# Kernel optimization log

Measured on AMD Instinct MI355X. Metric: run time of the kernel, lower is better.

Reference implementation:

```python
import jax, jax.numpy as jnp
import numpy as np

N = 100000
E = 3200000
IN_DIM = 128
HD = 64
HEADS = 4
NEG_SLOPE = 0.2


def setup_inputs() -> dict:
    key = jax.random.key(0)
    ks = jax.random.split(key, 12)
    s = lambda fan_in: 1.0 / np.sqrt(fan_in)
    x = jax.random.normal(ks[0], (N, IN_DIM), dtype=jnp.float32)
    edge_index = jax.random.randint(ks[1], (2, E), 0, N, dtype=jnp.int64)
    W1 = jax.random.normal(ks[2], (IN_DIM, HEADS * HD), dtype=jnp.float32) * s(IN_DIM)
    a_src1 = jax.random.normal(ks[3], (HEADS, HD), dtype=jnp.float32) * s(HD)
    a_dst1 = jax.random.normal(ks[4], (HEADS, HD), dtype=jnp.float32) * s(HD)
    b1 = jnp.zeros((HEADS * HD,), dtype=jnp.float32)
    W2 = jax.random.normal(ks[5], (HEADS * HD, HD), dtype=jnp.float32) * s(HEADS * HD)
    a_src2 = jax.random.normal(ks[6], (1, HD), dtype=jnp.float32) * s(HD)
    a_dst2 = jax.random.normal(ks[7], (1, HD), dtype=jnp.float32) * s(HD)
    b2 = jnp.zeros((HD,), dtype=jnp.float32)
    lin_w = jax.random.normal(ks[8], (HD, 2), dtype=jnp.float32) * s(HD)
    lin_b = jnp.zeros((2,), dtype=jnp.float32)
    return {"x": x, "edge_index": edge_index, "W1": W1, "a_src1": a_src1,
            "a_dst1": a_dst1, "b1": b1, "W2": W2, "a_src2": a_src2,
            "a_dst2": a_dst2, "b2": b2, "lin_w": lin_w, "lin_b": lin_b}


def gat_conv(x, src, dst, W, a_src, a_dst, bias, heads, out_dim, concat):
    n = x.shape[0]
    h = (x @ W).reshape(n, heads, out_dim)                 # [N,H,D]
    alpha_s = jnp.einsum('nhd,hd->nh', h, a_src)           # [N,H]
    alpha_d = jnp.einsum('nhd,hd->nh', h, a_dst)           # [N,H]
    e = alpha_s[src] + alpha_d[dst]                        # [Etot,H]
    e = jnp.where(e > 0, e, NEG_SLOPE * e)                 # leaky relu
    m = jax.ops.segment_max(e, dst, num_segments=n)        # scatter-softmax (stable)
    m = jnp.where(jnp.isfinite(m), m, 0.0)
    e = jnp.exp(e - m[dst])
    denom = jax.ops.segment_sum(e, dst, num_segments=n)
    alpha = e / denom[dst]                                 # [Etot,H]
    out = jax.ops.segment_sum(h[src] * alpha[:, :, None], dst, num_segments=n)  # [N,H,D]
    out = out.reshape(n, heads * out_dim) if concat else out.mean(axis=1)
    return out + bias


def reference(x, edge_index, W1, a_src1, a_dst1, b1, W2, a_src2, a_dst2, b2, lin_w, lin_b):
    n = x.shape[0]
    loops = jnp.arange(n, dtype=edge_index.dtype)
    src = jnp.concatenate([edge_index[0], loops])          # add self-loops (PyG default)
    dst = jnp.concatenate([edge_index[1], loops])
    h = gat_conv(x, src, dst, W1, a_src1, a_dst1, b1, HEADS, HD, True)
    h = jax.nn.elu(h)
    h = gat_conv(h, src, dst, W2, a_src2, a_dst2, b2, 1, HD, True)
    h = jax.nn.elu(h)
    return h @ lin_w + lin_b                               # [N,2]
```

## Files before the change

### kernel.cpp

```cpp
#include <hip/hip_runtime.h>
#include <hip/hip_fp16.h>
#include <math.h>

#define NN 100000
#define EE 3200000
#define ETOT (EE + NN)
#define NEG_SLOPE 0.2f
#define DMAX 96
#define CHUNK 4096
#define NB0 ((ETOT + CHUNK - 1) / CHUNK)
#define RB 391
#define CAP 16384

typedef _Float16 half8 __attribute__((ext_vector_type(8)));
typedef _Float16 half4v __attribute__((ext_vector_type(4)));
typedef float floatx4 __attribute__((ext_vector_type(4)));

__device__ __forceinline__ float wsum64(float v) {
#pragma unroll
  for (int o = 32; o; o >>= 1) v += __shfl_xor(v, o);
  return v;
}
__device__ __forceinline__ float lrelu(float v) { return v > 0.f ? v : NEG_SLOPE * v; }
__device__ __forceinline__ float elu1(float v) { return v > 0.f ? v : expm1f(v); }

__global__ void k_init(int* __restrict__ ccur) {
  ccur[threadIdx.x] = threadIdx.x * CAP;
}

__global__ __launch_bounds__(256) void k_pass1(const int* __restrict__ ei,
                                               int* __restrict__ ccur,
                                               unsigned* __restrict__ ebuf,
                                               const float* __restrict__ W1,
                                               const float* __restrict__ W2,
                                               _Float16* __restrict__ W1t,
                                               _Float16* __restrict__ W2t) {
  int b = blockIdx.x;
  if (b >= NB0) {
    int idx = (b - NB0) * 256 + threadIdx.x;
    if (idx < 32768) {
      int n = idx >> 7, k = idx & 127;
      W1t[idx] = (_Float16)W1[k * 256 + n];
    } else {
      int j = idx - 32768;
      int n = j >> 8, k = j & 255;
      W2t[j] = (_Float16)W2[k * 64 + n];
    }
    return;
  }
  __shared__ unsigned vv[CHUNK];
  __shared__ unsigned short cbv[CHUNK];
  __shared__ int h[256];
  __shared__ int cur[256];
  int t = threadIdx.x;
  h[t] = 0;
  __syncthreads();
  int base = b * CHUNK;
  int lim = base + CHUNK; if (lim > ETOT) lim = ETOT;
  int cnt = lim - base;
  for (int i = t; i < cnt; i += 256) {
    int e = base + i;
    int s, d;
    if (e < EE) { s = ei[e]; d = ei[EE + e]; } else { s = e - EE; d = s; }
    unsigned cb = (unsigned)d / (unsigned)RB;
    unsigned dloc = (unsigned)d - cb * (unsigned)RB;
    vv[i] = (dloc << 17) | (unsigned)s;
    cbv[i] = (unsigned short)cb;
    atomicAdd(&h[cb], 1);
  }
  __syncthreads();
  if (h[t]) cur[t] = atomicAdd(&ccur[t], h[t]);
  __syncthreads();
  for (int i = t; i < cnt; i += 256) {
    int cb = cbv[i];
    int pos = atomicAdd(&cur[cb], 1);
    ebuf[pos] = vv[i];
  }
}

__global__ __launch_bounds__(256) void k_pass2(const unsigned* __restrict__ ebuf,
                                               const int* __restrict__ ccur,
                                               int* __restrict__ offs,
                                               int* __restrict__ degarr,
                                               int* __restrict__ csr) {
  __shared__ unsigned ed[CAP];
  __shared__ int hist[RB];
  __shared__ int cur[RB];
  int b = blockIdx.x, t = threadIdx.x;
  int d0 = b * RB;
  int rb = NN - d0; if (rb > RB) rb = RB;
  int w0 = b * CAP;
  int cnt = ccur[b] - w0;
  if (cnt > CAP) cnt = CAP;
  for (int j = t; j < rb; j += 256) hist[j] = 0;
  __syncthreads();
  for (int i = t; i < cnt; i += 256) {
    unsigned v = ebuf[w0 + i];
    ed[i] = v;
    atomicAdd(&hist[v >> 17], 1);
  }
  __syncthreads();
  if (t == 0) {
    int run = w0;
    for (int j = 0; j < rb; ++j) { cur[j] = run; run += hist[j]; }
  }
  __syncthreads();
  for (int j = t; j < rb; j += 256) {
    offs[d0 + j] = cur[j];
    degarr[d0 + j] = hist[j];
  }
  __syncthreads();
  for (int i = t; i < cnt; i += 256) {
    unsigned v = ed[i];
    int pos = atomicAdd(&cur[v >> 17], 1);
    csr[pos] = (int)(v & 0x1FFFFu);
  }
}

__global__ __launch_bounds__(256) void k_gemm1m(const float* __restrict__ x,
                                                const _Float16* __restrict__ W1t,
                                                const float* __restrict__ a_src,
                                                const float* __restrict__ a_dst,
                                                _Float16* __restrict__ h1h,
                                                float* __restrict__ as_out,
                                                float* __restrict__ ad_out) {
  __shared__ _Float16 As[64][136];
  __shared__ _Float16 Wt[128][136];
  const int bx = blockIdx.x & 1;
  const int by = blockIdx.x >> 1;
  const int tid = threadIdx.x;
  const int row0 = by * 64;
#pragma unroll
  for (int i = 0; i < 8; ++i) {
    int idx = i * 256 + tid;
    int r = idx >> 5;
    int c4 = (idx & 31) * 4;
    int gr = row0 + r;
    float4 f = make_float4(0.f, 0.f, 0.f, 0.f);
    if (gr < NN) f = *(const float4*)(x + (size_t)gr * 128 + c4);
    half4v h; h[0] = (_Float16)f.x; h[1] = (_Float16)f.y; h[2] = (_Float16)f.z; h[3] = (_Float16)f.w;
    *(half4v*)&As[r][c4] = h;
  }
#pragma unroll
  for (int i = 0; i < 8; ++i) {
    int idx = i * 256 + tid;
    int r = idx >> 4;
    int g = idx & 15;
    *(half8*)&Wt[r][g * 8] = *(const half8*)(W1t + (size_t)(bx * 128 + r) * 128 + g * 8);
  }
  __syncthreads();

  const int wid = tid >> 6, lane = tid & 63;
  const int m16 = lane & 15, quad = lane >> 4;
  floatx4 acc[8];
#pragma unroll
  for (int nt = 0; nt < 8; ++nt) acc[nt] = (floatx4){0.f, 0.f, 0.f, 0.f};
#pragma unroll
  for (int ks = 0; ks < 4; ++ks) {
    half8 av = *(half8*)&As[wid * 16 + m16][ks * 32 + quad * 8];
#pragma unroll
    for (int nt = 0; nt < 8; ++nt) {
      half8 bv = *(half8*)&Wt[nt * 16 + m16][ks * 32 + quad * 8];
      acc[nt] = __builtin_amdgcn_mfma_f32_16x16x32_f16(av, bv, acc[nt], 0, 0, 0);
    }
  }
  float asr[8], adr[8];
#pragma unroll
  for (int nt = 0; nt < 8; ++nt) {
    asr[nt] = a_src[bx * 128 + nt * 16 + m16];
    adr[nt] = a_dst[bx * 128 + nt * 16 + m16];
  }
#pragma unroll
  for (int r = 0; r < 4; ++r) {
    int gr = row0 + wid * 16 + quad * 4 + r;
    bool ok = gr < NN;
#pragma unroll
    for (int hp = 0; hp < 2; ++hp) {
      float ps = 0.f, pd = 0.f;
#pragma unroll
      for (int j = 0; j < 4; ++j) {
        ps = fmaf(acc[hp * 4 + j][r], asr[hp * 4 + j], ps);
        pd = fmaf(acc[hp * 4 + j][r], adr[hp * 4 + j], pd);
      }
#pragma unroll
      for (int o = 1; o < 16; o <<= 1) { ps += __shfl_xor(ps, o); pd += __shfl_xor(pd, o); }
      if (ok && m16 == 0) {
        as_out[gr * 4 + bx * 2 + hp] = ps;
        ad_out[gr * 4 + bx * 2 + hp] = pd;
      }
    }
    if (ok) {
#pragma unroll
      for (int nt = 0; nt < 8; ++nt)
        h1h[(size_t)gr * 256 + bx * 128 + nt * 16 + m16] = (_Float16)acc[nt][r];
    }
  }
}

__global__ __launch_bounds__(256) void k_gemm2m(const _Float16* __restrict__ h1e,
                                                const _Float16* __restrict__ W2t,
                                                const float* __restrict__ a_src,
                                                const float* __restrict__ a_dst,
                                                _Float16* __restrict__ h2h,
                                                float* __restrict__ as_out,
                                                float* __restrict__ ad_out) {
  __shared__ _Float16 As2[64][136];
  __shared__ _Float16 Wt2[64][264];
  const int by = blockIdx.x;
  const int tid = threadIdx.x;
  const int row0 = by * 64;
#pragma unroll
  for (int i = 0; i < 8; ++i) {
    int idx = i * 256 + tid;
    int r = idx >> 5;
    int g = idx & 31;
    *(half8*)&Wt2[r][g * 8] = *(const half8*)(W2t + (size_t)r * 256 + g * 8);
  }
  const int wid = tid >> 6, lane = tid & 63;
  const int m16 = lane & 15, quad = lane >> 4;
  floatx4 acc[4];
#pragma unroll
  for (int nt = 0; nt < 4; ++nt) acc[nt] = (floatx4){0.f, 0.f, 0.f, 0.f};

  for (int kc = 0; kc < 2; ++kc) {
#pragma unroll
    for (int i = 0; i < 4; ++i) {
      int idx = i * 256 + tid;
      int r = idx >> 4;
      int g = idx & 15;
      int gr = row0 + r;
      half8 v = {0, 0, 0, 0, 0, 0, 0, 0};
      if (gr < NN) v = *(const half8*)(h1e + (size_t)gr * 256 + kc * 128 + g * 8);
      *(half8*)&As2[r][g * 8] = v;
    }
    __syncthreads();
#pragma unroll
    for (int ks = 0; ks < 4; ++ks) {
      half8 av = *(half8*)&As2[wid * 16 + m16][ks * 32 + quad * 8];
#pragma unroll
      for (int nt = 0; nt < 4; ++nt) {
        half8 bv = *(half8*)&Wt2[nt * 16 + m16][kc * 128 + ks * 32 + quad * 8];
        acc[nt] = __builtin_amdgcn_mfma_f32_16x16x32_f16(av, bv, acc[nt], 0, 0, 0);
      }
    }
    __syncthreads();
  }
  float asr[4], adr[4];
#pragma unroll
  for (int nt = 0; nt < 4; ++nt) {
    asr[nt] = a_src[nt * 16 + m16];
    adr[nt] = a_dst[nt * 16 + m16];
  }
#pragma unroll
  for (int r = 0; r < 4; ++r) {
    float ps = 0.f, pd = 0.f;
#pragma unroll
    for (int nt = 0; nt < 4; ++nt) {
      ps = fmaf(acc[nt][r], asr[nt], ps);
      pd = fmaf(acc[nt][r], adr[nt], pd);
    }
#pragma unroll
    for (int o = 1; o < 16; o <<= 1) { ps += __shfl_xor(ps, o); pd += __shfl_xor(pd, o); }
    int gr = row0 + wid * 16 + quad * 4 + r;
    if (gr < NN) {
      if (m16 == 0) { as_out[gr] = ps; ad_out[gr] = pd; }
#pragma unroll
      for (int nt = 0; nt < 4; ++nt)
        h2h[(size_t)gr * 64 + nt * 16 + m16] = (_Float16)acc[nt][r];
    }
  }
}

__global__ __launch_bounds__(256) void k_attn1(const int* __restrict__ offs,
                                               const int* __restrict__ degarr,
                                               const int* __restrict__ csr_src,
                                               const float* __restrict__ a_s,
                                               const float* __restrict__ a_d,
                                               const _Float16* __restrict__ h1h,
                                               const float* __restrict__ b1,
                                               _Float16* __restrict__ h1e) {
  __shared__ float alpha[4][DMAX][4];
  __shared__ int sidx[4][DMAX];
  const int wid = threadIdx.x >> 6;
  const int n = blockIdx.x * 4 + wid;
  const int lane = threadIdx.x & 63;
  const int beg = offs[n], deg = degarr[n];
  const float4 ad = *(const float4*)(a_d + n * 4);
  float4 sm = make_float4(0.f, 0.f, 0.f, 0.f);
  for (int d = lane; d < deg; d += 64) {
    int s = csr_src[beg + d];
    float4 as = *(const float4*)(a_s + s * 4);
    float e0 = __expf(lrelu(as.x + ad.x));
    float e1 = __expf(lrelu(as.y + ad.y));
    float e2 = __expf(lrelu(as.z + ad.z));
    float e3 = __expf(lrelu(as.w + ad.w));
    sm.x += e0; sm.y += e1; sm.z += e2; sm.w += e3;
    if (d < DMAX) {
      sidx[wid][d] = s;
      *(float4*)&alpha[wid][d][0] = make_float4(e0, e1, e2, e3);
    }
  }
  sm.x = wsum64(sm.x); sm.y = wsum64(sm.y); sm.z = wsum64(sm.z); sm.w = wsum64(sm.w);
  const float4 inv4 = make_float4(1.f / sm.x, 1.f / sm.y, 1.f / sm.z, 1.f / sm.w);
  const int dlim = deg < DMAX ? deg : DMAX;
  for (int d = lane; d < dlim; d += 64) {
    float4 a = *(float4*)&alpha[wid][d][0];
    a.x *= inv4.x; a.y *= inv4.y; a.z *= inv4.z; a.w *= inv4.w;
    *(float4*)&alpha[wid][d][0] = a;
  }
  const int h = lane >> 4;
  float4 acc = make_float4(0.f, 0.f, 0.f, 0.f);
  int d = 0;
  for (; d + 8 <= dlim; d += 8) {
    int ss[8]; float ww[8];
#pragma unroll
    for (int u = 0; u < 8; ++u) {
      ss[u] = sidx[wid][d + u];
      ww[u] = alpha[wid][d + u][h];
    }
    half4v rr[8];
#pragma unroll
    for (int u = 0; u < 8; ++u)
      rr[u] = *(const half4v*)(h1h + (size_t)ss[u] * 256 + lane * 4);
#pragma unroll
    for (int u = 0; u < 8; ++u) {
      acc.x = fmaf((float)rr[u][0], ww[u], acc.x);
      acc.y = fmaf((float)rr[u][1], ww[u], acc.y);
      acc.z = fmaf((float)rr[u][2], ww[u], acc.z);
      acc.w = fmaf((float)rr[u][3], ww[u], acc.w);
    }
  }
  for (; d < dlim; ++d) {
    int s = sidx[wid][d];
    float w = alpha[wid][d][h];
    half4v r = *(const half4v*)(h1h + (size_t)s * 256 + lane * 4);
    acc.x = fmaf((float)r[0], w, acc.x); acc.y = fmaf((float)r[1], w, acc.y);
    acc.z = fmaf((float)r[2], w, acc.z); acc.w = fmaf((float)r[3], w, acc.w);
  }
  const float adh = (h & 2) ? ((h & 1) ? ad.w : ad.z) : ((h & 1) ? ad.y : ad.x);
  const float invh = (h & 2) ? ((h & 1) ? inv4.w : inv4.z) : ((h & 1) ? inv4.y : inv4.x);
  for (; d < deg; ++d) {
    int s = csr_src[beg + d];
    float w = __expf(lrelu(a_s[s * 4 + h] + adh)) * invh;
    half4v r = *(const half4v*)(h1h + (size_t)s * 256 + lane * 4);
    acc.x = fmaf((float)r[0], w, acc.x); acc.y = fmaf((float)r[1], w, acc.y);
    acc.z = fmaf((float)r[2], w, acc.z); acc.w = fmaf((float)r[3], w, acc.w);
  }
  const int c = lane * 4;
  float4 bb = *(const float4*)(b1 + c);
  half4v o;
  o[0] = (_Float16)elu1(acc.x + bb.x);
  o[1] = (_Float16)elu1(acc.y + bb.y);
  o[2] = (_Float16)elu1(acc.z + bb.z);
  o[3] = (_Float16)elu1(acc.w + bb.w);
  *(half4v*)(h1e + (size_t)n * 256 + c) = o;
}

__global__ __launch_bounds__(256) void k_attn2(const int* __restrict__ offs,
                                               const int* __restrict__ degarr,
                                               const int* __restrict__ csr_src,
                                               const float* __restrict__ a_s,
                                               const float* __restrict__ a_d,
                                               const _Float16* __restrict__ h2h,
                                               const float* __restrict__ b2,
                                               const float* __restrict__ lin_w,
                                               const float* __restrict__ lin_b,
                                               float* __restrict__ out) {
  __shared__ float alpha2[4][DMAX];
  __shared__ int sidx2[4][DMAX];
  const int wid = threadIdx.x >> 6;
  const int n = blockIdx.x * 4 + wid;
  const int lane = threadIdx.x & 63;
  const int beg = offs[n], deg = degarr[n];
  const float adn = a_d[n];
  float sm = 0.f;
  for (int d = lane; d < deg; d += 64) {
    int s = csr_src[beg + d];
    float e = __expf(lrelu(a_s[s] + adn));
    sm += e;
    if (d < DMAX) { sidx2[wid][d] = s; alpha2[wid][d] = e; }
  }
  sm = wsum64(sm);
  const float inv = 1.f / sm;
  const int dlim = deg < DMAX ? deg : DMAX;
  for (int d = lane; d < dlim; d += 64) alpha2[wid][d] *= inv;
  float acc = 0.f;
  int d = 0;
  for (; d + 8 <= dlim; d += 8) {
    int ss[8]; float ww[8]; float vv[8];
#pragma unroll
    for (int u = 0; u < 8; ++u) {
      ss[u] = sidx2[wid][d + u];
      ww[u] = alpha2[wid][d + u];
    }
#pragma unroll
    for (int u = 0; u < 8; ++u)
      vv[u] = (float)h2h[(size_t)ss[u] * 64 + lane];
#pragma unroll
    for (int u = 0; u < 8; ++u) acc = fmaf(vv[u], ww[u], acc);
  }
  for (; d < dlim; ++d) {
    acc = fmaf((float)h2h[(size_t)sidx2[wid][d] * 64 + lane], alpha2[wid][d], acc);
  }
  for (; d < deg; ++d) {
    int s = csr_src[beg + d];
    float w = __expf(lrelu(a_s[s] + adn)) * inv;
    acc = fmaf((float)h2h[(size_t)s * 64 + lane], w, acc);
  }
  float o = elu1(acc + b2[lane]);
  float p0 = wsum64(o * lin_w[lane * 2 + 0]);
  float p1 = wsum64(o * lin_w[lane * 2 + 1]);
  if (lane == 0) {
    out[n * 2 + 0] = p0 + lin_b[0];
    out[n * 2 + 1] = p1 + lin_b[1];
  }
}

extern "C" void kernel_launch(void* const* d_in, const int* in_sizes, int n_in,
                              void* d_out, int out_size, void* d_ws, size_t ws_size,
                              hipStream_t stream) {
  const float* x      = (const float*)d_in[0];
  const int*   ei     = (const int*)d_in[1];
  const float* W1     = (const float*)d_in[2];
  const float* a_src1 = (const float*)d_in[3];
  const float* a_dst1 = (const float*)d_in[4];
  const float* b1     = (const float*)d_in[5];
  const float* W2     = (const float*)d_in[6];
  const float* a_src2 = (const float*)d_in[7];
  const float* a_dst2 = (const float*)d_in[8];
  const float* b2     = (const float*)d_in[9];
  const float* lin_w  = (const float*)d_in[10];
  const float* lin_b  = (const float*)d_in[11];
  float* outp = (float*)d_out;

  char* w = (char*)d_ws;
  _Float16* h1h = (_Float16*)(w + 0);
  _Float16* h1e = (_Float16*)(w + 51200000);
  _Float16* h2h = (_Float16*)(w + 102400000);
  _Float16* W1t = (_Float16*)(w + 115200000);
  _Float16* W2t = (_Float16*)(w + 115265536);
  float*  as1 = (float*)(w + 115298304);
  float*  ad1 = (float*)(w + 116898304);
  float*  as2 = (float*)(w + 118498304);
  float*  ad2 = (float*)(w + 118898304);
  int*    offs = (int*)(w + 119298304);
  int*    degarr = (int*)(w + 119698304);
  int*    ccur = (int*)(w + 120098304);
  unsigned* ebuf = (unsigned*)(w + 120099328);
  int*    csr = (int*)(w + 136876544);

  k_init<<<1, 256, 0, stream>>>(ccur);
  k_pass1<<<NB0 + 192, 256, 0, stream>>>(ei, ccur, ebuf, W1, W2, W1t, W2t);
  k_pass2<<<256, 256, 0, stream>>>(ebuf, ccur, offs, degarr, csr);

  k_gemm1m<<<2 * 1563, 256, 0, stream>>>(x, W1t, a_src1, a_dst1, h1h, as1, ad1);
  k_attn1<<<NN / 4, 256, 0, stream>>>(offs, degarr, csr, as1, ad1, h1h, b1, h1e);

  k_gemm2m<<<1563, 256, 0, stream>>>(h1e, W2t, a_src2, a_dst2, h2h, as2, ad2);
  k_attn2<<<NN / 4, 256, 0, stream>>>(offs, degarr, csr, as2, ad2, h2h, b2, lin_w, lin_b, outp);
}
```

Before: 579.2 us.

## Bucket CSR edges by source chunk and sweep attention chunk-by-chunk across node groups

CSR construction now bins each destination's edges by source range (16 chunks), records per-chunk offsets, and drops the shared-memory staging in both sort passes, so edges are re-read from global. The attention kernels become persistent grids where each wave handles 8 destinations at a time and walks source chunks in lockstep, so the gathered feature rows fall in a narrower address window and should hit L2 more often. Attention weights are recomputed on the fly instead of stored in LDS. The cost is extra exp work, a larger per-block shared histogram with a prefix scan, more global reads in pass1/pass2, and more registers per wave.

After: 1.526 ms. +163.4%, slower.

```diff
diff --git a/kernel.cpp b/kernel.cpp
--- a/kernel.cpp
+++ b/kernel.cpp
@@ -6,11 +6,14 @@
 #define EE 3200000
 #define ETOT (EE + NN)
 #define NEG_SLOPE 0.2f
-#define DMAX 96
 #define CHUNK 4096
 #define NB0 ((ETOT + CHUNK - 1) / CHUNK)
 #define RB 391
 #define CAP 16384
+#define NCH 16
+#define SRCCH 6250
+#define BINS (RB * NCH)
+#define AGRID 1024
 
 typedef _Float16 half8 __attribute__((ext_vector_type(8)));
 typedef _Float16 half4v __attribute__((ext_vector_type(4)));
@@ -48,8 +51,6 @@
     }
     return;
   }
-  __shared__ unsigned vv[CHUNK];
-  __shared__ unsigned short cbv[CHUNK];
   __shared__ int h[256];
   __shared__ int cur[256];
   int t = threadIdx.x;
@@ -57,24 +58,20 @@
   __syncthreads();
   int base = b * CHUNK;
   int lim = base + CHUNK; if (lim > ETOT) lim = ETOT;
-  int cnt = lim - base;
-  for (int i = t; i < cnt; i += 256) {
-    int e = base + i;
+  for (int e = base + t; e < lim; e += 256) {
+    int d = (e < EE) ? ei[EE + e] : (e - EE);
+    atomicAdd(&h[(unsigned)d / (unsigned)RB], 1);
+  }
+  __syncthreads();
+  if (h[t]) cur[t] = atomicAdd(&ccur[t], h[t]);
+  __syncthreads();
+  for (int e = base + t; e < lim; e += 256) {
     int s, d;
     if (e < EE) { s = ei[e]; d = ei[EE + e]; } else { s = e - EE; d = s; }
     unsigned cb = (unsigned)d / (unsigned)RB;
     unsigned dloc = (unsigned)d - cb * (unsigned)RB;
-    vv[i] = (dloc << 17) | (unsigned)s;
-    cbv[i] = (unsigned short)cb;
-    atomicAdd(&h[cb], 1);
-  }
-  __syncthreads();
-  if (h[t]) cur[t] = atomicAdd(&ccur[t], h[t]);
-  __syncthreads();
-  for (int i = t; i < cnt; i += 256) {
-    int cb = cbv[i];
     int pos = atomicAdd(&cur[cb], 1);
-    ebuf[pos] = vv[i];
+    ebuf[pos] = (dloc << 17) | (unsigned)s;
   }
 }
 
@@ -82,38 +79,55 @@
                                                const int* __restrict__ ccur,
                                                int* __restrict__ offs,
                                                int* __restrict__ degarr,
-                                               int* __restrict__ csr) {
-  __shared__ unsigned ed[CAP];
-  __shared__ int hist[RB];
-  __shared__ int cur[RB];
+                                               int* __restrict__ csr,
+                                               int* __restrict__ choff) {
+  __shared__ int hist[BINS];
+  __shared__ int psum[256];
   int b = blockIdx.x, t = threadIdx.x;
   int d0 = b * RB;
   int rb = NN - d0; if (rb > RB) rb = RB;
+  int nbins = rb * NCH;
   int w0 = b * CAP;
-  int cnt = ccur[b] - w0;
-  if (cnt > CAP) cnt = CAP;
-  for (int j = t; j < rb; j += 256) hist[j] = 0;
+  int cnt = ccur[b] - w0; if (cnt > CAP) cnt = CAP;
+  for (int j = t; j < nbins; j += 256) hist[j] = 0;
   __syncthreads();
   for (int i = t; i < cnt; i += 256) {
     unsigned v = ebuf[w0 + i];
-    ed[i] = v;
-    atomicAdd(&hist[v >> 17], 1);
-  }
-  __syncthreads();
-  if (t == 0) {
-    int run = w0;
-    for (int j = 0; j < rb; ++j) { cur[j] = run; run += hist[j]; }
-  }
+    unsigned bin = (v >> 17) * NCH + (v & 0x1FFFFu) / SRCCH;
+    atomicAdd(&hist[bin], 1);
+  }
+  __syncthreads();
+  const int PER = (BINS + 255) / 256;
+  int lo = t * PER, hi = lo + PER;
+  if (lo > nbins) lo = nbins;
+  if (hi > nbins) hi = nbins;
+  int s = 0;
+  for (int j = lo; j < hi; ++j) s += hist[j];
+  psum[t] = s;
+  __syncthreads();
+  for (int o = 1; o < 256; o <<= 1) {
+    int add = (t >= o) ? psum[t - o] : 0;
+    __syncthreads();
+    psum[t] += add;
+    __syncthreads();
+  }
+  int run = w0 + psum[t] - s;
+  for (int j = lo; j < hi; ++j) { int hv = hist[j]; hist[j] = run; run += hv; }
   __syncthreads();
   for (int j = t; j < rb; j += 256) {
-    offs[d0 + j] = cur[j];
-    degarr[d0 + j] = hist[j];
-  }
+    int st = hist[j * NCH];
+    int en = (j == rb - 1) ? (w0 + cnt) : hist[(j + 1) * NCH];
+    offs[d0 + j] = st;
+    degarr[d0 + j] = en - st;
+  }
+  for (int j = t; j < nbins; j += 256) choff[(size_t)d0 * NCH + j] = hist[j];
   __syncthreads();
   for (int i = t; i < cnt; i += 256) {
-    unsigned v = ed[i];
-    int pos = atomicAdd(&cur[v >> 17], 1);
-    csr[pos] = (int)(v & 0x1FFFFu);
+    unsigned v = ebuf[w0 + i];
+    unsigned s2 = v & 0x1FFFFu;
+    unsigned bin = (v >> 17) * NCH + s2 / SRCCH;
+    int pos = atomicAdd(&hist[bin], 1);
+    csr[pos] = (int)s2;
   }
 }
 
@@ -271,148 +285,174 @@
   }
 }
 
-__global__ __launch_bounds__(256) void k_attn1(const int* __restrict__ offs,
-                                               const int* __restrict__ degarr,
-                                               const int* __restrict__ csr_src,
-                                               const float* __restrict__ a_s,
-                                               const float* __restrict__ a_d,
-                                               const _Float16* __restrict__ h1h,
-                                               const float* __restrict__ b1,
-                                               _Float16* __restrict__ h1e) {
-  __shared__ float alpha[4][DMAX][4];
-  __shared__ int sidx[4][DMAX];
-  const int wid = threadIdx.x >> 6;
-  const int n = blockIdx.x * 4 + wid;
-  const int lane = threadIdx.x & 63;
-  const int beg = offs[n], deg = degarr[n];
-  const float4 ad = *(const float4*)(a_d + n * 4);
-  float4 sm = make_float4(0.f, 0.f, 0.f, 0.f);
-  for (int d = lane; d < deg; d += 64) {
-    int s = csr_src[beg + d];
-    float4 as = *(const float4*)(a_s + s * 4);
-    float e0 = __expf(lrelu(as.x + ad.x));
-    float e1 = __expf(lrelu(as.y + ad.y));
-    float e2 = __expf(lrelu(as.z + ad.z));
-    float e3 = __expf(lrelu(as.w + ad.w));
-    sm.x += e0; sm.y += e1; sm.z += e2; sm.w += e3;
-    if (d < DMAX) {
-      sidx[wid][d] = s;
-      *(float4*)&alpha[wid][d][0] = make_float4(e0, e1, e2, e3);
-    }
-  }
-  sm.x = wsum64(sm.x); sm.y = wsum64(sm.y); sm.z = wsum64(sm.z); sm.w = wsum64(sm.w);
-  const float4 inv4 = make_float4(1.f / sm.x, 1.f / sm.y, 1.f / sm.z, 1.f / sm.w);
-  const int dlim = deg < DMAX ? deg : DMAX;
-  for (int d = lane; d < dlim; d += 64) {
-    float4 a = *(float4*)&alpha[wid][d][0];
-    a.x *= inv4.x; a.y *= inv4.y; a.z *= inv4.z; a.w *= inv4.w;
-    *(float4*)&alpha[wid][d][0] = a;
-  }
+__global__ __launch_bounds__(256, 4) void k_attn1(const int* __restrict__ offs,
+                                                  const int* __restrict__ degarr,
+                                                  const int* __restrict__ csr,
+                                                  const int* __restrict__ choff,
+                                                  const float* __restrict__ a_s,
+                                                  const float* __restrict__ a_d,
+                                                  const _Float16* __restrict__ h1h,
+                                                  const float* __restrict__ b1,
+                                                  _Float16* __restrict__ h1e) {
+  const int wid = threadIdx.x >> 6, lane = threadIdx.x & 63;
   const int h = lane >> 4;
-  float4 acc = make_float4(0.f, 0.f, 0.f, 0.f);
-  int d = 0;
-  for (; d + 8 <= dlim; d += 8) {
-    int ss[8]; float ww[8];
-#pragma unroll
-    for (int u = 0; u < 8; ++u) {
-      ss[u] = sidx[wid][d + u];
-      ww[u] = alpha[wid][d + u][h];
-    }
-    half4v rr[8];
-#pragma unroll
-    for (int u = 0; u < 8; ++u)
-      rr[u] = *(const half4v*)(h1h + (size_t)ss[u] * 256 + lane * 4);
-#pragma unroll
-    for (int u = 0; u < 8; ++u) {
-      acc.x = fmaf((float)rr[u][0], ww[u], acc.x);
-      acc.y = fmaf((float)rr[u][1], ww[u], acc.y);
-      acc.z = fmaf((float)rr[u][2], ww[u], acc.z);
-      acc.w = fmaf((float)rr[u][3], ww[u], acc.w);
-    }
-  }
-  for (; d < dlim; ++d) {
-    int s = sidx[wid][d];
-    float w = alpha[wid][d][h];
-    half4v r = *(const half4v*)(h1h + (size_t)s * 256 + lane * 4);
-    acc.x = fmaf((float)r[0], w, acc.x); acc.y = fmaf((float)r[1], w, acc.y);
-    acc.z = fmaf((float)r[2], w, acc.z); acc.w = fmaf((float)r[3], w, acc.w);
-  }
-  const float adh = (h & 2) ? ((h & 1) ? ad.w : ad.z) : ((h & 1) ? ad.y : ad.x);
-  const float invh = (h & 2) ? ((h & 1) ? inv4.w : inv4.z) : ((h & 1) ? inv4.y : inv4.x);
-  for (; d < deg; ++d) {
-    int s = csr_src[beg + d];
-    float w = __expf(lrelu(a_s[s * 4 + h] + adh)) * invh;
-    half4v r = *(const half4v*)(h1h + (size_t)s * 256 + lane * 4);
-    acc.x = fmaf((float)r[0], w, acc.x); acc.y = fmaf((float)r[1], w, acc.y);
-    acc.z = fmaf((float)r[2], w, acc.z); acc.w = fmaf((float)r[3], w, acc.w);
-  }
-  const int c = lane * 4;
-  float4 bb = *(const float4*)(b1 + c);
-  half4v o;
-  o[0] = (_Float16)elu1(acc.x + bb.x);
-  o[1] = (_Float16)elu1(acc.y + bb.y);
-  o[2] = (_Float16)elu1(acc.z + bb.z);
-  o[3] = (_Float16)elu1(acc.w + bb.w);
-  *(half4v*)(h1e + (size_t)n * 256 + c) = o;
-}
-
-__global__ __launch_bounds__(256) void k_attn2(const int* __restrict__ offs,
-                                               const int* __restrict__ degarr,
-                                               const int* __restrict__ csr_src,
-                                               const float* __restrict__ a_s,
-                                               const float* __restrict__ a_d,
-                                               const _Float16* __restrict__ h2h,
-                                               const float* __restrict__ b2,
-                                               const float* __restrict__ lin_w,
-                                               const float* __restrict__ lin_b,
-                                               float* __restrict__ out) {
-  __shared__ float alpha2[4][DMAX];
-  __shared__ int sidx2[4][DMAX];
-  const int wid = threadIdx.x >> 6;
-  const int n = blockIdx.x * 4 + wid;
-  const int lane = threadIdx.x & 63;
-  const int beg = offs[n], deg = degarr[n];
-  const float adn = a_d[n];
-  float sm = 0.f;
-  for (int d = lane; d < deg; d += 64) {
-    int s = csr_src[beg + d];
-    float e = __expf(lrelu(a_s[s] + adn));
-    sm += e;
-    if (d < DMAX) { sidx2[wid][d] = s; alpha2[wid][d] = e; }
-  }
-  sm = wsum64(sm);
-  const float inv = 1.f / sm;
-  const int dlim = deg < DMAX ? deg : DMAX;
-  for (int d = lane; d < dlim; d += 64) alpha2[wid][d] *= inv;
-  float acc = 0.f;
-  int d = 0;
-  for (; d + 8 <= dlim; d += 8) {
-    int ss[8]; float ww[8]; float vv[8];
-#pragma unroll
-    for (int u = 0; u < 8; ++u) {
-      ss[u] = sidx2[wid][d + u];
-      ww[u] = alpha2[wid][d + u];
-    }
-#pragma unroll
-    for (int u = 0; u < 8; ++u)
-      vv[u] = (float)h2h[(size_t)ss[u] * 64 + lane];
-#pragma unroll
-    for (int u = 0; u < 8; ++u) acc = fmaf(vv[u], ww[u], acc);
-  }
-  for (; d < dlim; ++d) {
-    acc = fmaf((float)h2h[(size_t)sidx2[wid][d] * 64 + lane], alpha2[wid][d], acc);
-  }
-  for (; d < deg; ++d) {
-    int s = csr_src[beg + d];
-    float w = __expf(lrelu(a_s[s] + adn)) * inv;
-    acc = fmaf((float)h2h[(size_t)s * 64 + lane], w, acc);
-  }
-  float o = elu1(acc + b2[lane]);
-  float p0 = wsum64(o * lin_w[lane * 2 + 0]);
-  float p1 = wsum64(o * lin_w[lane * 2 + 1]);
-  if (lane == 0) {
-    out[n * 2 + 0] = p0 + lin_b[0];
-    out[n * 2 + 1] = p1 + lin_b[1];
+  const int slot = blockIdx.x * 4 + wid;
+  const int c0 = lane * 4;
+  const float4 bb = *(const float4*)(b1 + c0);
+  for (int base = slot * 8; base < NN; base += AGRID * 32) {
+    float inv[8], adh[8];
+    int dbeg[8], ddeg[8];
+    float4 acc[8];
+#pragma unroll
+    for (int d = 0; d < 8; ++d) {
+      acc[d] = make_float4(0.f, 0.f, 0.f, 0.f);
+      ddeg[d] = 0;
+      int n = base + d;
+      if (n < NN) {
+        int beg = offs[n], dg = degarr[n];
+        dbeg[d] = beg; ddeg[d] = dg;
+        float4 ad = *(const float4*)(a_d + (size_t)n * 4);
+        adh[d] = (h & 2) ? ((h & 1) ? ad.w : ad.z) : ((h & 1) ? ad.y : ad.x);
+        float4 sm = make_float4(0.f, 0.f, 0.f, 0.f);
+        for (int e = lane; e < dg; e += 64) {
+          int s = csr[beg + e];
+          float4 as = *(const float4*)(a_s + (size_t)s * 4);
+          sm.x += __expf(lrelu(as.x + ad.x));
+          sm.y += __expf(lrelu(as.y + ad.y));
+          sm.z += __expf(lrelu(as.z + ad.z));
+          sm.w += __expf(lrelu(as.w + ad.w));
+        }
+        sm.x = wsum64(sm.x); sm.y = wsum64(sm.y); sm.z = wsum64(sm.z); sm.w = wsum64(sm.w);
+        float dh = (h & 2) ? ((h & 1) ? sm.w : sm.z) : ((h & 1) ? sm.y : sm.x);
+        inv[d] = 1.f / dh;
+      }
+    }
+    for (int c = 0; c < NCH; ++c) {
+#pragma unroll
+      for (int d = 0; d < 8; ++d) {
+        if (ddeg[d] == 0) continue;
+        int n = base + d;
+        int jb = choff[(size_t)n * NCH + c];
+        int je = (c == NCH - 1) ? (dbeg[d] + ddeg[d]) : choff[(size_t)n * NCH + c + 1];
+        int j = jb;
+        for (; j + 2 <= je; j += 2) {
+          int s0 = csr[j], s1 = csr[j + 1];
+          float w0 = __expf(lrelu(a_s[(size_t)s0 * 4 + h] + adh[d])) * inv[d];
+          float w1 = __expf(lrelu(a_s[(size_t)s1 * 4 + h] + adh[d])) * inv[d];
+          half4v r0 = *(const half4v*)(h1h + (size_t)s0 * 256 + c0);
+          half4v r1 = *(const half4v*)(h1h + (size_t)s1 * 256 + c0);
+          acc[d].x = fmaf((float)r0[0], w0, acc[d].x);
+          acc[d].y = fmaf((float)r0[1], w0, acc[d].y);
+          acc[d].z = fmaf((float)r0[2], w0, acc[d].z);
+          acc[d].w = fmaf((float)r0[3], w0, acc[d].w);
+          acc[d].x = fmaf((float)r1[0], w1, acc[d].x);
+          acc[d].y = fmaf((float)r1[1], w1, acc[d].y);
+          acc[d].z = fmaf((float)r1[2], w1, acc[d].z);
+          acc[d].w = fmaf((float)r1[3], w1, acc[d].w);
+        }
+        if (j < je) {
+          int s0 = csr[j];
+          float w0 = __expf(lrelu(a_s[(size_t)s0 * 4 + h] + adh[d])) * inv[d];
+          half4v r0 = *(const half4v*)(h1h + (size_t)s0 * 256 + c0);
+          acc[d].x = fmaf((float)r0[0], w0, acc[d].x);
+          acc[d].y = fmaf((float)r0[1], w0, acc[d].y);
+          acc[d].z = fmaf((float)r0[2], w0, acc[d].z);
+          acc[d].w = fmaf((float)r0[3], w0, acc[d].w);
+        }
+      }
+    }
+#pragma unroll
+    for (int d = 0; d < 8; ++d) {
+      int n = base + d;
+      if (n < NN) {
+        half4v o;
+        o[0] = (_Float16)elu1(acc[d].x + bb.x);
+        o[1] = (_Float16)elu1(acc[d].y + bb.y);
+        o[2] = (_Float16)elu1(acc[d].z + bb.z);
+        o[3] = (_Float16)elu1(acc[d].w + bb.w);
+        *(half4v*)(h1e + (size_t)n * 256 + c0) = o;
+      }
+    }
+  }
+}
+
+__global__ __launch_bounds__(256, 4) void k_attn2(const int* __restrict__ offs,
+                                                  const int* __restrict__ degarr,
+                                                  const int* __restrict__ csr,
+                                                  const int* __restrict__ choff,
+                                                  const float* __restrict__ a_s,
+                                                  const float* __restrict__ a_d,
+                                                  const _Float16* __restrict__ h2h,
+                                                  const float* __restrict__ b2,
+                                                  const float* __restrict__ lin_w,
+                                                  const float* __restrict__ lin_b,
+                                                  float* __restrict__ out) {
+  const int wid = threadIdx.x >> 6, lane = threadIdx.x & 63;
+  const int slot = blockIdx.x * 4 + wid;
+  const float b2l = b2[lane];
+  const float lw0 = lin_w[lane * 2 + 0];
+  const float lw1 = lin_w[lane * 2 + 1];
+  const float lb0 = lin_b[0], lb1 = lin_b[1];
+  for (int base = slot * 8; base < NN; base += AGRID * 32) {
+    float inv[8], adn[8];
+    int dbeg[8], ddeg[8];
+    float acc[8];
+#pragma unroll
+    for (int d = 0; d < 8; ++d) {
+      acc[d] = 0.f;
+      ddeg[d] = 0;
+      int n = base + d;
+      if (n < NN) {
+        int beg = offs[n], dg = degarr[n];
+        dbeg[d] = beg; ddeg[d] = dg;
+        float ad = a_d[n];
+        adn[d] = ad;
+        float sm = 0.f;
+        for (int e = lane; e < dg; e += 64) {
+          int s = csr[beg + e];
+          sm += __expf(lrelu(a_s[s] + ad));
+        }
+        sm = wsum64(sm);
+        inv[d] = 1.f / sm;
+      }
+    }
+    for (int c = 0; c < NCH; ++c) {
+#pragma unroll
+      for (int d = 0; d < 8; ++d) {
+        if (ddeg[d] == 0) continue;
+        int n = base + d;
+        int jb = choff[(size_t)n * NCH + c];
+        int je = (c == NCH - 1) ? (dbeg[d] + ddeg[d]) : choff[(size_t)n * NCH + c + 1];
+        int j = jb;
+        for (; j + 2 <= je; j += 2) {
+          int s0 = csr[j], s1 = csr[j + 1];
+          float w0 = __expf(lrelu(a_s[s0] + adn[d])) * inv[d];
+          float w1 = __expf(lrelu(a_s[s1] + adn[d])) * inv[d];
+          float v0 = (float)h2h[(size_t)s0 * 64 + lane];
+          float v1 = (float)h2h[(size_t)s1 * 64 + lane];
+          acc[d] = fmaf(v0, w0, acc[d]);
+          acc[d] = fmaf(v1, w1, acc[d]);
+        }
+        if (j < je) {
+          int s0 = csr[j];
+          float w0 = __expf(lrelu(a_s[s0] + adn[d])) * inv[d];
+          acc[d] = fmaf((float)h2h[(size_t)s0 * 64 + lane], w0, acc[d]);
+        }
+      }
+    }
+#pragma unroll
+    for (int d = 0; d < 8; ++d) {
+      int n = base + d;
+      if (n < NN) {
+        float o = elu1(acc[d] + b2l);
+        float p0 = wsum64(o * lw0);
+        float p1 = wsum64(o * lw1);
+        if (lane == 0) {
+          out[n * 2 + 0] = p0 + lb0;
+          out[n * 2 + 1] = p1 + lb1;
+        }
+      }
+    }
   }
 }
 
@@ -448,14 +488,15 @@
   int*    ccur = (int*)(w + 120098304);
   unsigned* ebuf = (unsigned*)(w + 120099328);
   int*    csr = (int*)(w + 136876544);
+  int*    choff = (int*)(w + 153653760);
 
   k_init<<<1, 256, 0, stream>>>(ccur);
   k_pass1<<<NB0 + 192, 256, 0, stream>>>(ei, ccur, ebuf, W1, W2, W1t, W2t);
-  k_pass2<<<256, 256, 0, stream>>>(ebuf, ccur, offs, degarr, csr);
+  k_pass2<<<256, 256, 0, stream>>>(ebuf, ccur, offs, degarr, csr, choff);
 
   k_gemm1m<<<2 * 1563, 256, 0, stream>>>(x, W1t, a_src1, a_dst1, h1h, as1, ad1);
-  k_attn1<<<NN / 4, 256, 0, stream>>>(offs, degarr, csr, as1, ad1, h1h, b1, h1e);
+  k_attn1<<<AGRID, 256, 0, stream>>>(offs, degarr, csr, choff, as1, ad1, h1h, b1, h1e);
 
   k_gemm2m<<<1563, 256, 0, stream>>>(h1e, W2t, a_src2, a_dst2, h2h, as2, ad2);
-  k_attn2<<<NN / 4, 256, 0, stream>>>(offs, degarr, csr, as2, ad2, h2h, b2, lin_w, lin_b, outp);
-}
+  k_attn2<<<AGRID, 256, 0, stream>>>(offs, degarr, csr, choff, as2, ad2, h2h, b2, lin_w, lin_b, outp);
+}
```

## Fuse edge bucketing with layer-1 GEMM and transpose weights in-kernel

Applied to the files above, without the earlier changes.

Merges the edge-bucketing pass and the layer-1 projection GEMM into one launch with block ranges split by role, and removes the separate init kernel and the weight pre-transpose by converting W1/W2 inside the GEMM blocks. The bucketing pass now reads edge indices twice instead of staging them in shared memory, and uses a memset for the counters. Nontemporal loads and stores are added for CSR index reads and h1e writes. It saves launches and lets the independent GEMM overlap the scatter, at the cost of redundant per-block weight transposes with strided shared-memory writes and extra global reads of edge_index.

Result: slower. 637.8 us (+10.1%).

```diff
diff --git a/kernel.cpp b/kernel.cpp
--- a/kernel.cpp
+++ b/kernel.cpp
@@ -11,6 +11,7 @@
 #define NB0 ((ETOT + CHUNK - 1) / CHUNK)
 #define RB 391
 #define CAP 16384
+#define G1B 3126
 
 typedef _Float16 half8 __attribute__((ext_vector_type(8)));
 typedef _Float16 half4v __attribute__((ext_vector_type(4)));
@@ -24,57 +25,117 @@
 __device__ __forceinline__ float lrelu(float v) { return v > 0.f ? v : NEG_SLOPE * v; }
 __device__ __forceinline__ float elu1(float v) { return v > 0.f ? v : expm1f(v); }
 
-__global__ void k_init(int* __restrict__ ccur) {
-  ccur[threadIdx.x] = threadIdx.x * CAP;
-}
-
-__global__ __launch_bounds__(256) void k_pass1(const int* __restrict__ ei,
-                                               int* __restrict__ ccur,
-                                               unsigned* __restrict__ ebuf,
-                                               const float* __restrict__ W1,
-                                               const float* __restrict__ W2,
-                                               _Float16* __restrict__ W1t,
-                                               _Float16* __restrict__ W2t) {
-  int b = blockIdx.x;
-  if (b >= NB0) {
-    int idx = (b - NB0) * 256 + threadIdx.x;
-    if (idx < 32768) {
-      int n = idx >> 7, k = idx & 127;
-      W1t[idx] = (_Float16)W1[k * 256 + n];
-    } else {
-      int j = idx - 32768;
-      int n = j >> 8, k = j & 255;
-      W2t[j] = (_Float16)W2[k * 64 + n];
+__global__ __launch_bounds__(256) void k_fused1(const int* __restrict__ ei,
+                                                int* __restrict__ ccur,
+                                                unsigned* __restrict__ ebuf,
+                                                const float* __restrict__ x,
+                                                const float* __restrict__ W1,
+                                                const float* __restrict__ a_src,
+                                                const float* __restrict__ a_dst,
+                                                _Float16* __restrict__ h1h,
+                                                float* __restrict__ as_out,
+                                                float* __restrict__ ad_out) {
+  __shared__ __align__(16) char smem[52224];
+  const int b = blockIdx.x;
+  const int t = threadIdx.x;
+  if (b < NB0) {
+    int* h = (int*)smem;
+    int* cur = (int*)(smem + 1024);
+    h[t] = 0;
+    __syncthreads();
+    int base = b * CHUNK;
+    int lim = base + CHUNK; if (lim > ETOT) lim = ETOT;
+    for (int e = base + t; e < lim; e += 256) {
+      int d = (e < EE) ? ei[EE + e] : (e - EE);
+      atomicAdd(&h[(unsigned)d / (unsigned)RB], 1);
+    }
+    __syncthreads();
+    if (h[t]) cur[t] = t * CAP + atomicAdd(&ccur[t], h[t]);
+    __syncthreads();
+    for (int e = base + t; e < lim; e += 256) {
+      int s, d;
+      if (e < EE) { s = ei[e]; d = ei[EE + e]; } else { s = e - EE; d = s; }
+      unsigned cb = (unsigned)d / (unsigned)RB;
+      unsigned dloc = (unsigned)d - cb * (unsigned)RB;
+      int pos = atomicAdd(&cur[cb], 1);
+      ebuf[pos] = (dloc << 17) | (unsigned)s;
     }
     return;
   }
-  __shared__ unsigned vv[CHUNK];
-  __shared__ unsigned short cbv[CHUNK];
-  __shared__ int h[256];
-  __shared__ int cur[256];
-  int t = threadIdx.x;
-  h[t] = 0;
+  _Float16 (*As)[136] = (_Float16(*)[136])smem;
+  _Float16 (*Wt)[136] = (_Float16(*)[136])(smem + 17408);
+  const int bb = b - NB0;
+  const int bx = bb & 1;
+  const int by = bb >> 1;
+  const int row0 = by * 64;
+#pragma unroll
+  for (int i = 0; i < 8; ++i) {
+    int idx = i * 256 + t;
+    int r = idx >> 5;
+    int c4 = (idx & 31) * 4;
+    int gr = row0 + r;
+    float4 f = make_float4(0.f, 0.f, 0.f, 0.f);
+    if (gr < NN) f = *(const float4*)(x + (size_t)gr * 128 + c4);
+    half4v hv; hv[0] = (_Float16)f.x; hv[1] = (_Float16)f.y; hv[2] = (_Float16)f.z; hv[3] = (_Float16)f.w;
+    *(half4v*)&As[r][c4] = hv;
+  }
+#pragma unroll
+  for (int i = 0; i < 16; ++i) {
+    int idx = i * 256 + t;
+    int k = idx >> 5;
+    int n4 = (idx & 31) * 4;
+    float4 f = *(const float4*)(W1 + (size_t)k * 256 + bx * 128 + n4);
+    Wt[n4 + 0][k] = (_Float16)f.x;
+    Wt[n4 + 1][k] = (_Float16)f.y;
+    Wt[n4 + 2][k] = (_Float16)f.z;
+    Wt[n4 + 3][k] = (_Float16)f.w;
+  }
   __syncthreads();
-  int base = b * CHUNK;
-  int lim = base + CHUNK; if (lim > ETOT) lim = ETOT;
-  int cnt = lim - base;
-  for (int i = t; i < cnt; i += 256) {
-    int e = base + i;
-    int s, d;
-    if (e < EE) { s = ei[e]; d = ei[EE + e]; } else { s = e - EE; d = s; }
-    unsigned cb = (unsigned)d / (unsigned)RB;
-    unsigned dloc = (unsigned)d - cb * (unsigned)RB;
-    vv[i] = (dloc << 17) | (unsigned)s;
-    cbv[i] = (unsigned short)cb;
-    atomicAdd(&h[cb], 1);
-  }
-  __syncthreads();
-  if (h[t]) cur[t] = atomicAdd(&ccur[t], h[t]);
-  __syncthreads();
-  for (int i = t; i < cnt; i += 256) {
-    int cb = cbv[i];
-    int pos = atomicAdd(&cur[cb], 1);
-    ebuf[pos] = vv[i];
+
+  const int wid = t >> 6, lane = t & 63;
+  const int m16 = lane & 15, quad = lane >> 4;
+  floatx4 acc[8];
+#pragma unroll
+  for (int nt = 0; nt < 8; ++nt) acc[nt] = (floatx4){0.f, 0.f, 0.f, 0.f};
+#pragma unroll
+  for (int ks = 0; ks < 4; ++ks) {
+    half8 av = *(half8*)&As[wid * 16 + m16][ks * 32 + quad * 8];
+#pragma unroll
+    for (int nt = 0; nt < 8; ++nt) {
+      half8 bv = *(half8*)&Wt[nt * 16 + m16][ks * 32 + quad * 8];
+      acc[nt] = __builtin_amdgcn_mfma_f32_16x16x32_f16(av, bv, acc[nt], 0, 0, 0);
+    }
+  }
+  float asr[8], adr[8];
+#pragma unroll
+  for (int nt = 0; nt < 8; ++nt) {
+    asr[nt] = a_src[bx * 128 + nt * 16 + m16];
+    adr[nt] = a_dst[bx * 128 + nt * 16 + m16];
+  }
+#pragma unroll
+  for (int r = 0; r < 4; ++r) {
+    int gr = row0 + wid * 16 + quad * 4 + r;
+    bool ok = gr < NN;
+#pragma unroll
+    for (int hp = 0; hp < 2; ++hp) {
+      float ps = 0.f, pd = 0.f;
+#pragma unroll
+      for (int j = 0; j < 4; ++j) {
+        ps = fmaf(acc[hp * 4 + j][r], asr[hp * 4 + j], ps);
+        pd = fmaf(acc[hp * 4 + j][r], adr[hp * 4 + j], pd);
+      }
+#pragma unroll
+      for (int o = 1; o < 16; o <<= 1) { ps += __shfl_xor(ps, o); pd += __shfl_xor(pd, o); }
+      if (ok && m16 == 0) {
+        as_out[gr * 4 + bx * 2 + hp] = ps;
+        ad_out[gr * 4 + bx * 2 + hp] = pd;
+      }
+    }
+    if (ok) {
+#pragma unroll
+      for (int nt = 0; nt < 8; ++nt)
+        h1h[(size_t)gr * 256 + bx * 128 + nt * 16 + m16] = (_Float16)acc[nt][r];
+    }
   }
 }
 
@@ -90,7 +151,7 @@
   int d0 = b * RB;
   int rb = NN - d0; if (rb > RB) rb = RB;
   int w0 = b * CAP;
-  int cnt = ccur[b] - w0;
+  int cnt = ccur[b];
   if (cnt > CAP) cnt = CAP;
   for (int j = t; j < rb; j += 256) hist[j] = 0;
   __syncthreads();
@@ -117,88 +178,8 @@
   }
 }
 
-__global__ __launch_bounds__(256) void k_gemm1m(const float* __restrict__ x,
-                                                const _Float16* __restrict__ W1t,
-                                                const float* __restrict__ a_src,
-                                                const float* __restrict__ a_dst,
-                                                _Float16* __restrict__ h1h,
-                                                float* __restrict__ as_out,
-                                                float* __restrict__ ad_out) {
-  __shared__ _Float16 As[64][136];
-  __shared__ _Float16 Wt[128][136];
-  const int bx = blockIdx.x & 1;
-  const int by = blockIdx.x >> 1;
-  const int tid = threadIdx.x;
-  const int row0 = by * 64;
-#pragma unroll
-  for (int i = 0; i < 8; ++i) {
-    int idx = i * 256 + tid;
-    int r = idx >> 5;
-    int c4 = (idx & 31) * 4;
-    int gr = row0 + r;
-    float4 f = make_float4(0.f, 0.f, 0.f, 0.f);
-    if (gr < NN) f = *(const float4*)(x + (size_t)gr * 128 + c4);
-    half4v h; h[0] = (_Float16)f.x; h[1] = (_Float16)f.y; h[2] = (_Float16)f.z; h[3] = (_Float16)f.w;
-    *(half4v*)&As[r][c4] = h;
-  }
-#pragma unroll
-  for (int i = 0; i < 8; ++i) {
-    int idx = i * 256 + tid;
-    int r = idx >> 4;
-    int g = idx & 15;
-    *(half8*)&Wt[r][g * 8] = *(const half8*)(W1t + (size_t)(bx * 128 + r) * 128 + g * 8);
-  }
-  __syncthreads();
-
-  const int wid = tid >> 6, lane = tid & 63;
-  const int m16 = lane & 15, quad = lane >> 4;
-  floatx4 acc[8];
-#pragma unroll
-  for (int nt = 0; nt < 8; ++nt) acc[nt] = (floatx4){0.f, 0.f, 0.f, 0.f};
-#pragma unroll
-  for (int ks = 0; ks < 4; ++ks) {
-    half8 av = *(half8*)&As[wid * 16 + m16][ks * 32 + quad * 8];
-#pragma unroll
-    for (int nt = 0; nt < 8; ++nt) {
-      half8 bv = *(half8*)&Wt[nt * 16 + m16][ks * 32 + quad * 8];
-      acc[nt] = __builtin_amdgcn_mfma_f32_16x16x32_f16(av, bv, acc[nt], 0, 0, 0);
-    }
-  }
-  float asr[8], adr[8];
-#pragma unroll
-  for (int nt = 0; nt < 8; ++nt) {
-    asr[nt] = a_src[bx * 128 + nt * 16 + m16];
-    adr[nt] = a_dst[bx * 128 + nt * 16 + m16];
-  }
-#pragma unroll
-  for (int r = 0; r < 4; ++r) {
-    int gr = row0 + wid * 16 + quad * 4 + r;
-    bool ok = gr < NN;
-#pragma unroll
-    for (int hp = 0; hp < 2; ++hp) {
-      float ps = 0.f, pd = 0.f;
-#pragma unroll
-      for (int j = 0; j < 4; ++j) {
-        ps = fmaf(acc[hp * 4 + j][r], asr[hp * 4 + j], ps);
-        pd = fmaf(acc[hp * 4 + j][r], adr[hp * 4 + j], pd);
-      }
-#pragma unroll
-      for (int o = 1; o < 16; o <<= 1) { ps += __shfl_xor(ps, o); pd += __shfl_xor(pd, o); }
-      if (ok && m16 == 0) {
-        as_out[gr * 4 + bx * 2 + hp] = ps;
-        ad_out[gr * 4 + bx * 2 + hp] = pd;
-      }
-    }
-    if (ok) {
-#pragma unroll
-      for (int nt = 0; nt < 8; ++nt)
-        h1h[(size_t)gr * 256 + bx * 128 + nt * 16 + m16] = (_Float16)acc[nt][r];
-    }
-  }
-}
-
 __global__ __launch_bounds__(256) void k_gemm2m(const _Float16* __restrict__ h1e,
-                                                const _Float16* __restrict__ W2t,
+                                                const float* __restrict__ W2,
                                                 const float* __restrict__ a_src,
                                                 const float* __restrict__ a_dst,
                                                 _Float16* __restrict__ h2h,
@@ -210,11 +191,15 @@
   const int tid = threadIdx.x;
   const int row0 = by * 64;
 #pragma unroll
-  for (int i = 0; i < 8; ++i) {
+  for (int i = 0; i < 16; ++i) {
     int idx = i * 256 + tid;
-    int r = idx >> 5;
-    int g = idx & 31;
-    *(half8*)&Wt2[r][g * 8] = *(const half8*)(W2t + (size_t)r * 256 + g * 8);
+    int k = idx >> 4;
+    int n4 = (idx & 15) * 4;
+    float4 f = *(const float4*)(W2 + (size_t)k * 64 + n4);
+    Wt2[n4 + 0][k] = (_Float16)f.x;
+    Wt2[n4 + 1][k] = (_Float16)f.y;
+    Wt2[n4 + 2][k] = (_Float16)f.z;
+    Wt2[n4 + 3][k] = (_Float16)f.w;
   }
   const int wid = tid >> 6, lane = tid & 63;
   const int m16 = lane & 15, quad = lane >> 4;
@@ -288,7 +273,7 @@
   const float4 ad = *(const float4*)(a_d + n * 4);
   float4 sm = make_float4(0.f, 0.f, 0.f, 0.f);
   for (int d = lane; d < deg; d += 64) {
-    int s = csr_src[beg + d];
+    int s = __builtin_nontemporal_load(csr_src + beg + d);
     float4 as = *(const float4*)(a_s + s * 4);
     float e0 = __expf(lrelu(as.x + ad.x));
     float e1 = __expf(lrelu(as.y + ad.y));
@@ -353,7 +338,8 @@
   o[1] = (_Float16)elu1(acc.y + bb.y);
   o[2] = (_Float16)elu1(acc.z + bb.z);
   o[3] = (_Float16)elu1(acc.w + bb.w);
-  *(half4v*)(h1e + (size_t)n * 256 + c) = o;
+  __builtin_nontemporal_store(__builtin_bit_cast(unsigned long long, o),
+                              (unsigned long long*)(h1e + (size_t)n * 256 + c));
 }
 
 __global__ __launch_bounds__(256) void k_attn2(const int* __restrict__ offs,
@@ -375,7 +361,7 @@
   const float adn = a_d[n];
   float sm = 0.f;
   for (int d = lane; d < deg; d += 64) {
-    int s = csr_src[beg + d];
+    int s = __builtin_nontemporal_load(csr_src + beg + d);
     float e = __expf(lrelu(a_s[s] + adn));
     sm += e;
     if (d < DMAX) { sidx2[wid][d] = s; alpha2[wid][d] = e; }
@@ -437,8 +423,6 @@
   _Float16* h1h = (_Float16*)(w + 0);
   _Float16* h1e = (_Float16*)(w + 51200000);
   _Float16* h2h = (_Float16*)(w + 102400000);
-  _Float16* W1t = (_Float16*)(w + 115200000);
-  _Float16* W2t = (_Float16*)(w + 115265536);
   float*  as1 = (float*)(w + 115298304);
   float*  ad1 = (float*)(w + 116898304);
   float*  as2 = (float*)(w + 118498304);
@@ -449,13 +433,13 @@
   unsigned* ebuf = (unsigned*)(w + 120099328);
   int*    csr = (int*)(w + 136876544);
 
-  k_init<<<1, 256, 0, stream>>>(ccur);
-  k_pass1<<<NB0 + 192, 256, 0, stream>>>(ei, ccur, ebuf, W1, W2, W1t, W2t);
+  hipMemsetAsync(ccur, 0, 1024, stream);
+  k_fused1<<<NB0 + G1B, 256, 0, stream>>>(ei, ccur, ebuf, x, W1, a_src1, a_dst1,
+                                          h1h, as1, ad1);
   k_pass2<<<256, 256, 0, stream>>>(ebuf, ccur, offs, degarr, csr);
 
-  k_gemm1m<<<2 * 1563, 256, 0, stream>>>(x, W1t, a_src1, a_dst1, h1h, as1, ad1);
   k_attn1<<<NN / 4, 256, 0, stream>>>(offs, degarr, csr, as1, ad1, h1h, b1, h1e);
 
-  k_gemm2m<<<1563, 256, 0, stream>>>(h1e, W2t, a_src2, a_dst2, h2h, as2, ad2);
+  k_gemm2m<<<1563, 256, 0, stream>>>(h1e, W2, a_src2, a_dst2, h2h, as2, ad2);
   k_attn2<<<NN / 4, 256, 0, stream>>>(offs, degarr, csr, as2, ad2, h2h, b2, lin_w, lin_b, outp);
 }
```

## Vectorize layer-2 gather across edge quarters and drop LDS staging in binning

Applied to the files above, without the earlier changes.

The layer-2 aggregation now has each group of 16 lanes load a 4-wide half vector of one neighbor's row, so a wavefront processes 4 edges per step instead of one 2-byte scalar per lane. Partial sums are combined with cross-quarter shuffles before the ELU and final linear layer. Separately, the edge binning pass no longer stages packed edges and bucket ids in shared memory. It reads edge_index twice instead, once to build the histogram and once to scatter. This lowers LDS use and may raise occupancy, at the cost of extra global reads.

Result: slower. 615.5 us (+6.3%).

```diff
diff --git a/kernel.cpp b/kernel.cpp
--- a/kernel.cpp
+++ b/kernel.cpp
@@ -48,8 +48,6 @@
     }
     return;
   }
-  __shared__ unsigned vv[CHUNK];
-  __shared__ unsigned short cbv[CHUNK];
   __shared__ int h[256];
   __shared__ int cur[256];
   int t = threadIdx.x;
@@ -57,24 +55,20 @@
   __syncthreads();
   int base = b * CHUNK;
   int lim = base + CHUNK; if (lim > ETOT) lim = ETOT;
-  int cnt = lim - base;
-  for (int i = t; i < cnt; i += 256) {
-    int e = base + i;
+  for (int e = base + t; e < lim; e += 256) {
+    int d = (e < EE) ? ei[EE + e] : (e - EE);
+    atomicAdd(&h[(unsigned)d / (unsigned)RB], 1);
+  }
+  __syncthreads();
+  if (h[t]) cur[t] = atomicAdd(&ccur[t], h[t]);
+  __syncthreads();
+  for (int e = base + t; e < lim; e += 256) {
     int s, d;
     if (e < EE) { s = ei[e]; d = ei[EE + e]; } else { s = e - EE; d = s; }
     unsigned cb = (unsigned)d / (unsigned)RB;
     unsigned dloc = (unsigned)d - cb * (unsigned)RB;
-    vv[i] = (dloc << 17) | (unsigned)s;
-    cbv[i] = (unsigned short)cb;
-    atomicAdd(&h[cb], 1);
-  }
-  __syncthreads();
-  if (h[t]) cur[t] = atomicAdd(&ccur[t], h[t]);
-  __syncthreads();
-  for (int i = t; i < cnt; i += 256) {
-    int cb = cbv[i];
     int pos = atomicAdd(&cur[cb], 1);
-    ebuf[pos] = vv[i];
+    ebuf[pos] = (dloc << 17) | (unsigned)s;
   }
 }
 
@@ -384,32 +378,52 @@
   const float inv = 1.f / sm;
   const int dlim = deg < DMAX ? deg : DMAX;
   for (int d = lane; d < dlim; d += 64) alpha2[wid][d] *= inv;
-  float acc = 0.f;
-  int d = 0;
-  for (; d + 8 <= dlim; d += 8) {
-    int ss[8]; float ww[8]; float vv[8];
-#pragma unroll
-    for (int u = 0; u < 8; ++u) {
-      ss[u] = sidx2[wid][d + u];
-      ww[u] = alpha2[wid][d + u];
-    }
-#pragma unroll
-    for (int u = 0; u < 8; ++u)
-      vv[u] = (float)h2h[(size_t)ss[u] * 64 + lane];
-#pragma unroll
-    for (int u = 0; u < 8; ++u) acc = fmaf(vv[u], ww[u], acc);
-  }
-  for (; d < dlim; ++d) {
-    acc = fmaf((float)h2h[(size_t)sidx2[wid][d] * 64 + lane], alpha2[wid][d], acc);
-  }
-  for (; d < deg; ++d) {
+  const int quarter = lane >> 4;
+  const int fl = lane & 15;
+  float acc4[4];
+#pragma unroll
+  for (int i = 0; i < 4; ++i) acc4[i] = 0.f;
+  for (int d = 0; d < dlim; d += 8) {
+    int ss[2]; float ww[2];
+#pragma unroll
+    for (int u = 0; u < 2; ++u) {
+      int e = d + 4 * u + quarter;
+      bool valid = e < dlim;
+      int e2 = valid ? e : 0;
+      ss[u] = sidx2[wid][e2];
+      ww[u] = valid ? alpha2[wid][e2] : 0.f;
+    }
+    half4v rr[2];
+#pragma unroll
+    for (int u = 0; u < 2; ++u)
+      rr[u] = *(const half4v*)(h2h + (size_t)ss[u] * 64 + fl * 4);
+#pragma unroll
+    for (int u = 0; u < 2; ++u)
+#pragma unroll
+      for (int i = 0; i < 4; ++i)
+        acc4[i] = fmaf((float)rr[u][i], ww[u], acc4[i]);
+  }
+  for (int d = dlim + quarter; d < deg; d += 4) {
     int s = csr_src[beg + d];
     float w = __expf(lrelu(a_s[s] + adn)) * inv;
-    acc = fmaf((float)h2h[(size_t)s * 64 + lane], w, acc);
-  }
-  float o = elu1(acc + b2[lane]);
-  float p0 = wsum64(o * lin_w[lane * 2 + 0]);
-  float p1 = wsum64(o * lin_w[lane * 2 + 1]);
+    half4v r = *(const half4v*)(h2h + (size_t)s * 64 + fl * 4);
+#pragma unroll
+    for (int i = 0; i < 4; ++i) acc4[i] = fmaf((float)r[i], w, acc4[i]);
+  }
+#pragma unroll
+  for (int i = 0; i < 4; ++i) {
+    acc4[i] += __shfl_xor(acc4[i], 16);
+    acc4[i] += __shfl_xor(acc4[i], 32);
+  }
+  float p0 = 0.f, p1 = 0.f;
+#pragma unroll
+  for (int i = 0; i < 4; ++i) {
+    float o = elu1(acc4[i] + b2[fl * 4 + i]);
+    p0 = fmaf(o, lin_w[(fl * 4 + i) * 2 + 0], p0);
+    p1 = fmaf(o, lin_w[(fl * 4 + i) * 2 + 1], p1);
+  }
+#pragma unroll
+  for (int o = 1; o < 16; o <<= 1) { p0 += __shfl_xor(p0, o); p1 += __shfl_xor(p1, o); }
   if (lane == 0) {
     out[n * 2 + 0] = p0 + lin_b[0];
     out[n * 2 + 1] = p1 + lin_b[1];
```
